# Performance work log

Hardware: AMD Instinct MI355X
Metric: run time of the kernel (lower is better)

The kernel has to match this reference:

```python
import jax, jax.numpy as jnp
import numpy as np

B, S, HID, NH = 8, 1024, 1024, 16
DH = HID // NH
ZERO = 1e-8  # undefined repo constant, assumed small epsilon


def setup_inputs() -> dict:
    key = jax.random.key(0)
    ks = jax.random.split(key, 14)
    sc = 1.0 / np.sqrt(HID)
    inp = {
        "Q": jax.random.normal(ks[0], (B, S, HID), jnp.float32),
        "K": jax.random.normal(ks[1], (B, S, HID), jnp.float32),
        "V": jax.random.normal(ks[2], (B, S, HID), jnp.float32),
        "Q_mask": jax.random.randint(ks[3], (B, S), 0, 2).astype(jnp.float32),
        "K_mask": jax.random.randint(ks[4], (B, S), 0, 2).astype(jnp.float32),
        "Wq": jax.random.normal(ks[5], (HID, HID), jnp.float32) * sc,
        "bq": jnp.zeros((HID,), jnp.float32),
        "Wk": jax.random.normal(ks[6], (HID, HID), jnp.float32) * sc,
        "bk": jnp.zeros((HID,), jnp.float32),
        "Wv": jax.random.normal(ks[7], (HID, HID), jnp.float32) * sc,
        "bv": jnp.zeros((HID,), jnp.float32),
        "Wo": jax.random.normal(ks[8], (HID, HID), jnp.float32) * sc,
        "bo": jnp.zeros((HID,), jnp.float32),
    }
    return inp


def _heads(x):  # [B,S,HID] -> [B,NH,S,DH]
    b, s, _ = x.shape
    return x.reshape(b, s, NH, DH).transpose(0, 2, 1, 3)


def reference(Q, K, V, Q_mask, K_mask, Wq, bq, Wk, bk, Wv, bv, Wo, bo):
    q = _heads(Q @ Wq.T + bq)
    k = _heads(K @ Wk.T + bk)
    v = _heads(V @ Wv.T + bv)
    # NOTE: original divides by head_size**(-0.5) == multiply by sqrt(DH)
    scores = jnp.einsum("bhqd,bhkd->bhqk", q, k) / (DH ** (-0.5))
    mask = Q_mask[:, :, None] * K_mask[:, None, :]  # [B,Sq,Sk]
    probs = jax.nn.softmax(scores, axis=-1)
    probs = jnp.where(mask[:, None, :, :] == 0, 0.0, probs)
    probs = probs / jnp.sum(probs + ZERO, axis=-1, keepdims=True)
    ctx = jnp.einsum("bhqk,bhkd->bqhd", probs, v).reshape(Q.shape[0], Q.shape[1], HID)
    return ctx @ Wo.T + bo
```

## Files before the change

### kernel.cpp

```cpp
#include <hip/hip_runtime.h>
#include <math.h>

constexpr int Bc   = 8;
constexpr int Sc   = 1024;
constexpr int HIDc = 1024;
constexpr int NHc  = 16;
constexpr int DHc  = 64;
constexpr int Mc   = Bc * Sc;
constexpr int Kc2  = 1024;
constexpr float SCALE    = 8.0f;
constexpr float EPS_TERM = 1024.0f * 1e-8f;

typedef short s16x8 __attribute__((ext_vector_type(8)));
typedef float f32x4 __attribute__((ext_vector_type(4)));

__device__ __forceinline__ ushort f2bf(float f) {
  unsigned u = __float_as_uint(f);
  u += 0x7FFFu + ((u >> 16) & 1u);
  return (ushort)(u >> 16);
}
__device__ __forceinline__ float bf2f(ushort h) {
  return __uint_as_float(((unsigned)h) << 16);
}
__device__ __forceinline__ unsigned pk2bf(float a, float b) {
  return (unsigned)f2bf(a) | ((unsigned)f2bf(b) << 16);
}

__device__ __forceinline__ void gl_lds16(const ushort* g, ushort* l) {
  __builtin_amdgcn_global_load_lds(
      (const __attribute__((address_space(1))) void*)g,
      (__attribute__((address_space(3))) void*)l, 16, 0, 0);
}

__device__ __forceinline__ void split8(const float4 v0, const float4 v1,
                                       s16x8& hi, s16x8& lo) {
  const float f[8] = {v0.x, v0.y, v0.z, v0.w, v1.x, v1.y, v1.z, v1.w};
  ushort h[8], l[8];
#pragma unroll
  for (int i = 0; i < 8; i++) {
    h[i] = f2bf(f[i]);
    l[i] = f2bf(f[i] - bf2f(h[i]));
  }
#pragma unroll
  for (int i = 0; i < 8; i++) { hi[i] = (short)h[i]; lo[i] = (short)l[i]; }
}

__global__ __launch_bounds__(256) void cvt_weights(
    const float4* __restrict__ Wq, const float4* __restrict__ Wk,
    const float4* __restrict__ Wv, const float4* __restrict__ Wo,
    ushort4* __restrict__ Wqh, ushort4* __restrict__ Wql,
    ushort4* __restrict__ Wkh, ushort4* __restrict__ Wkl,
    ushort4* __restrict__ Wvh, ushort4* __restrict__ Woh, int n4w)
{
  const int bpseg = n4w / 256;
  const int seg   = blockIdx.x / bpseg;
  const int li    = (blockIdx.x - seg * bpseg) * 256 + threadIdx.x;
  if (li >= n4w) return;
  if (seg == 0) {
    const float4 v = Wq[li];
    ushort4 h, l;
    h.x = f2bf(v.x); l.x = f2bf(v.x - bf2f(h.x));
    h.y = f2bf(v.y); l.y = f2bf(v.y - bf2f(h.y));
    h.z = f2bf(v.z); l.z = f2bf(v.z - bf2f(h.z));
    h.w = f2bf(v.w); l.w = f2bf(v.w - bf2f(h.w));
    Wqh[li] = h; Wql[li] = l;
  } else if (seg == 1) {
    const float4 v = Wk[li];
    ushort4 h, l;
    h.x = f2bf(v.x); l.x = f2bf(v.x - bf2f(h.x));
    h.y = f2bf(v.y); l.y = f2bf(v.y - bf2f(h.y));
    h.z = f2bf(v.z); l.z = f2bf(v.z - bf2f(h.z));
    h.w = f2bf(v.w); l.w = f2bf(v.w - bf2f(h.w));
    Wkh[li] = h; Wkl[li] = l;
  } else {
    const float4 v = (seg == 2) ? Wv[li] : Wo[li];
    ushort4 h;
    h.x = f2bf(v.x); h.y = f2bf(v.y); h.z = f2bf(v.z); h.w = f2bf(v.w);
    if (seg == 2) Wvh[li] = h; else Woh[li] = h;
  }
}

__global__ __launch_bounds__(256, 3) void qkv_gemm(
    const float* __restrict__ Qf, const float* __restrict__ Kf,
    const float* __restrict__ Vf,
    const ushort* __restrict__ Wqh, const ushort* __restrict__ Wql,
    const ushort* __restrict__ Wkh, const ushort* __restrict__ Wkl,
    const ushort* __restrict__ Wvh,
    const float* __restrict__ bq, const float* __restrict__ bk,
    const float* __restrict__ bv,
    ushort* __restrict__ qhi, ushort* __restrict__ qlo,
    ushort* __restrict__ khi, ushort* __restrict__ klo,
    ushort* __restrict__ vt)
{
  __shared__ ushort AhL[4096];
  __shared__ ushort BhL[4096];
  __shared__ ushort AlL[4096];
  __shared__ ushort BlL[4096];

  const int z = blockIdx.z;
  const bool split = (z < 2);
  const float*  Af = (z == 0) ? Qf : (z == 1) ? Kf : Vf;
  const ushort* Bh = (z == 0) ? Wqh : (z == 1) ? Wkh : Wvh;
  const ushort* Bl = (z == 0) ? Wql : Wkl;
  const float* bias = (z == 0) ? bq : (z == 1) ? bk : bv;

  const int t    = threadIdx.x;
  const int w    = t >> 6;
  const int ln   = t & 63;
  const int col  = ln & 15;
  const int quad = ln >> 4;
  const int wm   = w >> 1, wn = w & 1;
  const int m0   = blockIdx.y * 128;
  const int n0   = blockIdx.x * 128;

  f32x4 acc[4][4] = {};

  const int sA = w * 128;

  for (int k0 = 0; k0 < Kc2; k0 += 32) {
    float4 av[2][2];
#pragma unroll
    for (int j = 0; j < 2; j++) {
      const int s = sA + j * 64 + ln;
      const int r = s & 127, c = s >> 7;
      const float4* ga = (const float4*)(Af + (size_t)(m0 + r) * Kc2 + k0 + c * 8);
      av[j][0] = ga[0];
      av[j][1] = ga[1];
    }

    __syncthreads();

#pragma unroll
    for (int j = 0; j < 2; j++) {
      const int s = sA + j * 64 + ln;
      const int r = s & 127, c = s >> 7;
      const size_t goB = (size_t)(n0 + r) * Kc2 + k0 + c * 8;
      gl_lds16(Bh + goB, &BhL[(size_t)(sA + j * 64) * 8]);
      if (split) gl_lds16(Bl + goB, &BlL[(size_t)(sA + j * 64) * 8]);
    }
#pragma unroll
    for (int j = 0; j < 2; j++) {
      const int s = sA + j * 64 + ln;
      s16x8 hi, lo;
      split8(av[j][0], av[j][1], hi, lo);
      *(s16x8*)&AhL[(size_t)s * 8] = hi;
      if (split) *(s16x8*)&AlL[(size_t)s * 8] = lo;
    }
    __syncthreads();

    s16x8 a_h[4], b_h[4], a_l[4], b_l[4];
#pragma unroll
    for (int i = 0; i < 4; i++) {
      const int ai = (quad * 128 + wm * 64 + i * 16 + col) * 8;
      const int bi = (quad * 128 + wn * 64 + i * 16 + col) * 8;
      a_h[i] = *(const s16x8*)&AhL[ai];
      b_h[i] = *(const s16x8*)&BhL[bi];
      if (split) {
        a_l[i] = *(const s16x8*)&AlL[ai];
        b_l[i] = *(const s16x8*)&BlL[bi];
      }
    }
#pragma unroll
    for (int i = 0; i < 4; i++)
#pragma unroll
      for (int jj = 0; jj < 4; jj++) {
        acc[i][jj] = __builtin_amdgcn_mfma_f32_16x16x32_bf16(a_h[i], b_h[jj], acc[i][jj], 0, 0, 0);
        if (split) {
          acc[i][jj] = __builtin_amdgcn_mfma_f32_16x16x32_bf16(a_h[i], b_l[jj], acc[i][jj], 0, 0, 0);
          acc[i][jj] = __builtin_amdgcn_mfma_f32_16x16x32_bf16(a_l[i], b_h[jj], acc[i][jj], 0, 0, 0);
        }
      }
  }

  const int mb = m0 + wm * 64;
  const int nb = n0 + wn * 64;
  ushort* Ch = (z == 0) ? qhi : khi;
  ushort* Cl = (z == 0) ? qlo : klo;
#pragma unroll
  for (int i = 0; i < 4; i++)
#pragma unroll
    for (int jj = 0; jj < 4; jj++) {
      const int n  = nb + jj * 16 + col;
      const float bvv = bias[n];
#pragma unroll
      for (int r = 0; r < 4; r++) {
        const int m   = mb + i * 16 + quad * 4 + r;
        const float v = acc[i][jj][r] + bvv;
        const int b_ = m >> 10, s = m & (Sc - 1);
        const int h_ = n >> 6,  d = n & (DHc - 1);
        if (split) {
          const size_t off = (((size_t)b_ * NHc + h_) * Sc + s) * DHc + d;
          const ushort hb = f2bf(v);
          Ch[off] = hb;
          Cl[off] = f2bf(v - bf2f(hb));
        } else {
          const size_t off = (((size_t)b_ * NHc + h_) * DHc + d) * Sc + s;
          vt[off] = f2bf(v);
        }
      }
    }
}

__global__ __launch_bounds__(256, 3) void o_gemm(
    const ushort* __restrict__ Ag, const ushort* __restrict__ Bg,
    const float* __restrict__ bias, float* __restrict__ C)
{
  __shared__ ushort AhL[4096];
  __shared__ ushort BhL[4096];

  const int t    = threadIdx.x;
  const int w    = t >> 6;
  const int ln   = t & 63;
  const int col  = ln & 15;
  const int quad = ln >> 4;
  const int wm   = w >> 1, wn = w & 1;
  const int m0   = blockIdx.y * 128;
  const int n0   = blockIdx.x * 128;

  f32x4 acc[4][4] = {};
  const int sA = w * 128;

  for (int k0 = 0; k0 < Kc2; k0 += 32) {
    __syncthreads();
#pragma unroll
    for (int j = 0; j < 2; j++) {
      const int s = sA + j * 64 + ln;
      const int r = s & 127, c = s >> 7;
      gl_lds16(Ag + (size_t)(m0 + r) * Kc2 + k0 + c * 8, &AhL[(size_t)(sA + j * 64) * 8]);
      gl_lds16(Bg + (size_t)(n0 + r) * Kc2 + k0 + c * 8, &BhL[(size_t)(sA + j * 64) * 8]);
    }
    __syncthreads();

    s16x8 a_h[4], b_h[4];
#pragma unroll
    for (int i = 0; i < 4; i++) {
      a_h[i] = *(const s16x8*)&AhL[(quad * 128 + wm * 64 + i * 16 + col) * 8];
      b_h[i] = *(const s16x8*)&BhL[(quad * 128 + wn * 64 + i * 16 + col) * 8];
    }
#pragma unroll
    for (int i = 0; i < 4; i++)
#pragma unroll
      for (int jj = 0; jj < 4; jj++)
        acc[i][jj] = __builtin_amdgcn_mfma_f32_16x16x32_bf16(a_h[i], b_h[jj], acc[i][jj], 0, 0, 0);
  }

  const int mb = m0 + wm * 64;
  const int nb = n0 + wn * 64;
#pragma unroll
  for (int i = 0; i < 4; i++)
#pragma unroll
    for (int jj = 0; jj < 4; jj++) {
      const int n  = nb + jj * 16 + col;
      const float bvv = bias[n];
#pragma unroll
      for (int r = 0; r < 4; r++) {
        const int m = mb + i * 16 + quad * 4 + r;
        C[(size_t)m * HIDc + n] = acc[i][jj][r] + bvv;
      }
    }
}

constexpr int LDP = 72;

__global__ __launch_bounds__(256, 4) void attn_mfma(
    const ushort* __restrict__ qhi, const ushort* __restrict__ qlo,
    const ushort* __restrict__ khi, const ushort* __restrict__ klo,
    const ushort* __restrict__ vt,  const float* __restrict__ Qm,
    const float* __restrict__ Km,   ushort* __restrict__ ctx)
{
  __shared__ ushort KhiL[4096];
  __shared__ ushort KloL[4096];
  __shared__ ushort VtL [4096];
  __shared__ ushort PmL [64 * LDP];
  __shared__ float  kmL[64];

  const int t    = threadIdx.x;
  const int w    = t >> 6;
  const int ln   = t & 63;
  const int col  = ln & 15;
  const int quad = ln >> 4;

  const int id  = blockIdx.x;
  const int xcd = id & 7;
  const int j   = id >> 3;
  const int bh  = xcd * 16 + (j >> 4);
  const int qt  = j & 15;
  const int b   = bh >> 4;
  const int h   = bh & 15;

  const int qbase = qt * 64 + w * 16;
  const size_t headoff = (size_t)bh * Sc * DHc;

  s16x8 qh0, qh1, ql0, ql1;
  {
    const size_t ro = headoff + (size_t)(qbase + col) * DHc + quad * 8;
    qh0 = *(const s16x8*)(qhi + ro);
    qh1 = *(const s16x8*)(qhi + ro + 32);
    ql0 = *(const s16x8*)(qlo + ro);
    ql1 = *(const s16x8*)(qlo + ro + 32);
  }

  f32x4 OT[4] = {{0,0,0,0},{0,0,0,0},{0,0,0,0},{0,0,0,0}};
  float mrow = -INFINITY;
  float Zp = 0.0f, Zmp = 0.0f;

  for (int k0 = 0; k0 < Sc; k0 += 64) {
    __syncthreads();
#pragma unroll
    for (int jj = 0; jj < 2; jj++) {
      const int c = jj * 4 + w;
      const size_t gk = headoff + (size_t)(k0 + ln) * DHc + c * 8;
      const size_t gv = headoff + (size_t)ln * Sc + k0 + c * 8;
      gl_lds16(khi + gk, &KhiL[c * 512]);
      gl_lds16(klo + gk, &KloL[c * 512]);
      gl_lds16(vt  + gv, &VtL [c * 512]);
    }
    if (t < 64) kmL[t] = Km[b * Sc + k0 + t];
    __syncthreads();

    float s[4][4];
#pragma unroll
    for (int ks = 0; ks < 4; ks++) {
      const int base0 = (quad * 64 + ks * 16 + col) * 8;
      const int base1 = ((quad + 4) * 64 + ks * 16 + col) * 8;
      const s16x8 kh0 = *(const s16x8*)&KhiL[base0];
      const s16x8 kh1 = *(const s16x8*)&KhiL[base1];
      const s16x8 kl0 = *(const s16x8*)&KloL[base0];
      const s16x8 kl1 = *(const s16x8*)&KloL[base1];
      f32x4 a = {0,0,0,0};
      a = __builtin_amdgcn_mfma_f32_16x16x32_bf16(kh0, qh0, a, 0, 0, 0);
      a = __builtin_amdgcn_mfma_f32_16x16x32_bf16(kh1, qh1, a, 0, 0, 0);
      a = __builtin_amdgcn_mfma_f32_16x16x32_bf16(kh0, ql0, a, 0, 0, 0);
      a = __builtin_amdgcn_mfma_f32_16x16x32_bf16(kh1, ql1, a, 0, 0, 0);
      a = __builtin_amdgcn_mfma_f32_16x16x32_bf16(kl0, qh0, a, 0, 0, 0);
      a = __builtin_amdgcn_mfma_f32_16x16x32_bf16(kl1, qh1, a, 0, 0, 0);
#pragma unroll
      for (int r = 0; r < 4; r++) s[ks][r] = a[r] * SCALE;
    }

    float tmax = s[0][0];
#pragma unroll
    for (int ks = 0; ks < 4; ks++)
#pragma unroll
      for (int r = 0; r < 4; r++) tmax = fmaxf(tmax, s[ks][r]);
    tmax = fmaxf(tmax, __shfl_xor(tmax, 16, 64));
    tmax = fmaxf(tmax, __shfl_xor(tmax, 32, 64));

    const float mn    = fmaxf(mrow, tmax);
    const float alpha = __expf(mrow - mn);
    mrow = mn;

    float ps = 0.0f, pms = 0.0f;
    const int prow = (w * 16 + col) * LDP;
#pragma unroll
    for (int ks = 0; ks < 4; ks++) {
      const float4 km4 = *(const float4*)&kmL[ks * 16 + quad * 4];
      const float p0 = __expf(s[ks][0] - mn), p1 = __expf(s[ks][1] - mn);
      const float p2 = __expf(s[ks][2] - mn), p3 = __expf(s[ks][3] - mn);
      const float q0 = p0 * km4.x, q1 = p1 * km4.y, q2 = p2 * km4.z, q3 = p3 * km4.w;
      ps  += (p0 + p1) + (p2 + p3);
      pms += (q0 + q1) + (q2 + q3);
      uint2 pv;
      pv.x = pk2bf(q0, q1);
      pv.y = pk2bf(q2, q3);
      *(uint2*)&PmL[prow + ks * 16 + quad * 4] = pv;
    }
    Zp  = Zp  * alpha + ps;
    Zmp = Zmp * alpha + pms;
#pragma unroll
    for (int dt = 0; dt < 4; dt++) OT[dt] *= alpha;

    const s16x8 p0 = *(const s16x8*)&PmL[prow + quad * 8];
    const s16x8 p1 = *(const s16x8*)&PmL[prow + 32 + quad * 8];
#pragma unroll
    for (int dt = 0; dt < 4; dt++) {
      const s16x8 a0 = *(const s16x8*)&VtL[(quad * 64 + dt * 16 + col) * 8];
      const s16x8 a1 = *(const s16x8*)&VtL[((quad + 4) * 64 + dt * 16 + col) * 8];
      OT[dt] = __builtin_amdgcn_mfma_f32_16x16x32_bf16(a0, p0, OT[dt], 0, 0, 0);
      OT[dt] = __builtin_amdgcn_mfma_f32_16x16x32_bf16(a1, p1, OT[dt], 0, 0, 0);
    }
  }

  Zp  += __shfl_xor(Zp,  16, 64);  Zp  += __shfl_xor(Zp,  32, 64);
  Zmp += __shfl_xor(Zmp, 16, 64);  Zmp += __shfl_xor(Zmp, 32, 64);

  const int q     = qbase + col;
  const float qmv = Qm[b * Sc + q];
  const float rden = (qmv != 0.0f) ? 1.0f / (Zmp + EPS_TERM * Zp) : 0.0f;

  ushort* crow = ctx + (size_t)(b * Sc + q) * HIDc + h * DHc + quad * 4;
#pragma unroll
  for (int dt = 0; dt < 4; dt++) {
    uint2 ov;
    ov.x = pk2bf(OT[dt][0] * rden, OT[dt][1] * rden);
    ov.y = pk2bf(OT[dt][2] * rden, OT[dt][3] * rden);
    *(uint2*)(crow + dt * 16) = ov;
  }
}

extern "C" void kernel_launch(void* const* d_in, const int* in_sizes, int n_in,
                              void* d_out, int out_size, void* d_ws, size_t ws_size,
                              hipStream_t stream)
{
  const float* Q  = (const float*)d_in[0];
  const float* K  = (const float*)d_in[1];
  const float* V  = (const float*)d_in[2];
  const float* Qm = (const float*)d_in[3];
  const float* Km = (const float*)d_in[4];
  const float* Wq = (const float*)d_in[5];
  const float* bq = (const float*)d_in[6];
  const float* Wk = (const float*)d_in[7];
  const float* bk = (const float*)d_in[8];
  const float* Wv = (const float*)d_in[9];
  const float* bv = (const float*)d_in[10];
  const float* Wo = (const float*)d_in[11];
  const float* bo = (const float*)d_in[12];
  float* out = (float*)d_out;

  const size_t NEL = (size_t)Mc * HIDc;
  const size_t WEL = (size_t)HIDc * HIDc;

  ushort* Wqh = (ushort*)d_ws;
  ushort* Wql = Wqh + WEL;
  ushort* Wkh = Wql + WEL;
  ushort* Wkl = Wkh + WEL;
  ushort* Wvh = Wkl + WEL;
  ushort* Woh = Wvh + WEL;
  ushort* qhi = Woh + WEL;
  ushort* qlo = qhi + NEL;
  ushort* khi = qlo + NEL;
  ushort* klo = khi + NEL;
  ushort* vt  = klo + NEL;
  ushort* ctx = vt  + NEL;

  const int n4w = (int)(WEL / 4);

  cvt_weights<<<4 * (n4w / 256), 256, 0, stream>>>(
      (const float4*)Wq, (const float4*)Wk, (const float4*)Wv, (const float4*)Wo,
      (ushort4*)Wqh, (ushort4*)Wql, (ushort4*)Wkh, (ushort4*)Wkl,
      (ushort4*)Wvh, (ushort4*)Woh, n4w);

  dim3 gqkv(HIDc / 128, Mc / 128, 3);
  qkv_gemm<<<gqkv, 256, 0, stream>>>(Q, K, V,
      Wqh, Wql, Wkh, Wkl, Wvh, bq, bk, bv, qhi, qlo, khi, klo, vt);

  attn_mfma<<<Bc * NHc * (Sc / 64), 256, 0, stream>>>(qhi, qlo, khi, klo, vt, Qm, Km, ctx);

  dim3 gg(HIDc / 128, Mc / 128);
  o_gemm<<<gg, 256, 0, stream>>>(ctx, Woh, bo, out);
}
```

Measured before the change: 524.2 us.

## Switch attention and output GEMM to fp16, drop K low split, remap blocks

Q/K/V projection outputs, attention probabilities, context and Wo now use fp16 instead of bf16. K is stored as a single fp16 value, so the K-low buffer and two of the six score MFMAs per step are removed, which also cuts LDS use and global loads. Occupancy is raised to 6 blocks per CU. The QKV and O GEMM grids are flattened to 1-D with a swizzled block-to-tile mapping that spreads work across XCDs. The risk is fp16 overflow or precision loss in scores and outputs, which a split-K scheme previously protected against.

```diff
diff --git a/kernel.cpp b/kernel.cpp
--- a/kernel.cpp
+++ b/kernel.cpp
@@ -22,8 +22,16 @@
 __device__ __forceinline__ float bf2f(ushort h) {
   return __uint_as_float(((unsigned)h) << 16);
 }
-__device__ __forceinline__ unsigned pk2bf(float a, float b) {
-  return (unsigned)f2bf(a) | ((unsigned)f2bf(b) << 16);
+__device__ __forceinline__ ushort f2h(float f) {
+  _Float16 h = (_Float16)f;
+  return *(ushort*)&h;
+}
+__device__ __forceinline__ float h2f(ushort u) {
+  _Float16 h = *(_Float16*)&u;
+  return (float)h;
+}
+__device__ __forceinline__ unsigned pk2h(float a, float b) {
+  return (unsigned)f2h(a) | ((unsigned)f2h(b) << 16);
 }
 
 __device__ __forceinline__ void gl_lds16(const ushort* g, ushort* l) {
@@ -72,11 +80,16 @@
     h.z = f2bf(v.z); l.z = f2bf(v.z - bf2f(h.z));
     h.w = f2bf(v.w); l.w = f2bf(v.w - bf2f(h.w));
     Wkh[li] = h; Wkl[li] = l;
-  } else {
-    const float4 v = (seg == 2) ? Wv[li] : Wo[li];
+  } else if (seg == 2) {
+    const float4 v = Wv[li];
     ushort4 h;
     h.x = f2bf(v.x); h.y = f2bf(v.y); h.z = f2bf(v.z); h.w = f2bf(v.w);
-    if (seg == 2) Wvh[li] = h; else Woh[li] = h;
+    Wvh[li] = h;
+  } else {
+    const float4 v = Wo[li];
+    ushort4 h;
+    h.x = f2h(v.x); h.y = f2h(v.y); h.z = f2h(v.z); h.w = f2h(v.w);
+    Woh[li] = h;
   }
 }
 
@@ -89,15 +102,20 @@
     const float* __restrict__ bq, const float* __restrict__ bk,
     const float* __restrict__ bv,
     ushort* __restrict__ qhi, ushort* __restrict__ qlo,
-    ushort* __restrict__ khi, ushort* __restrict__ klo,
-    ushort* __restrict__ vt)
+    ushort* __restrict__ kf,  ushort* __restrict__ vt)
 {
   __shared__ ushort AhL[4096];
   __shared__ ushort BhL[4096];
   __shared__ ushort AlL[4096];
   __shared__ ushort BlL[4096];
 
-  const int z = blockIdx.z;
+  const int lin = blockIdx.x;
+  const int wk  = (lin & 7) * 192 + (lin >> 3);
+  const int z   = wk >> 9;
+  const int rem = wk & 511;
+  const int m0  = (rem >> 3) * 128;
+  const int n0  = (rem & 7) * 128;
+
   const bool split = (z < 2);
   const float*  Af = (z == 0) ? Qf : (z == 1) ? Kf : Vf;
   const ushort* Bh = (z == 0) ? Wqh : (z == 1) ? Wkh : Wvh;
@@ -110,11 +128,8 @@
   const int col  = ln & 15;
   const int quad = ln >> 4;
   const int wm   = w >> 1, wn = w & 1;
-  const int m0   = blockIdx.y * 128;
-  const int n0   = blockIdx.x * 128;
 
   f32x4 acc[4][4] = {};
-
   const int sA = w * 128;
 
   for (int k0 = 0; k0 < Kc2; k0 += 32) {
@@ -174,8 +189,6 @@
 
   const int mb = m0 + wm * 64;
   const int nb = n0 + wn * 64;
-  ushort* Ch = (z == 0) ? qhi : khi;
-  ushort* Cl = (z == 0) ? qlo : klo;
 #pragma unroll
   for (int i = 0; i < 4; i++)
 #pragma unroll
@@ -188,14 +201,17 @@
         const float v = acc[i][jj][r] + bvv;
         const int b_ = m >> 10, s = m & (Sc - 1);
         const int h_ = n >> 6,  d = n & (DHc - 1);
-        if (split) {
+        if (z == 0) {
           const size_t off = (((size_t)b_ * NHc + h_) * Sc + s) * DHc + d;
-          const ushort hb = f2bf(v);
-          Ch[off] = hb;
-          Cl[off] = f2bf(v - bf2f(hb));
+          const ushort hb = f2h(v);
+          qhi[off] = hb;
+          qlo[off] = f2h(v - h2f(hb));
+        } else if (z == 1) {
+          const size_t off = (((size_t)b_ * NHc + h_) * Sc + s) * DHc + d;
+          kf[off] = f2h(v);
         } else {
           const size_t off = (((size_t)b_ * NHc + h_) * DHc + d) * Sc + s;
-          vt[off] = f2bf(v);
+          vt[off] = f2h(v);
         }
       }
     }
@@ -208,14 +224,17 @@
   __shared__ ushort AhL[4096];
   __shared__ ushort BhL[4096];
 
+  const int lin = blockIdx.x;
+  const int wk  = (lin & 7) * 64 + (lin >> 3);
+  const int m0  = (wk >> 3) * 128;
+  const int n0  = (wk & 7) * 128;
+
   const int t    = threadIdx.x;
   const int w    = t >> 6;
   const int ln   = t & 63;
   const int col  = ln & 15;
   const int quad = ln >> 4;
   const int wm   = w >> 1, wn = w & 1;
-  const int m0   = blockIdx.y * 128;
-  const int n0   = blockIdx.x * 128;
 
   f32x4 acc[4][4] = {};
   const int sA = w * 128;
@@ -241,7 +260,7 @@
     for (int i = 0; i < 4; i++)
 #pragma unroll
       for (int jj = 0; jj < 4; jj++)
-        acc[i][jj] = __builtin_amdgcn_mfma_f32_16x16x32_bf16(a_h[i], b_h[jj], acc[i][jj], 0, 0, 0);
+        acc[i][jj] = __builtin_amdgcn_mfma_f32_16x16x32_f16(a_h[i], b_h[jj], acc[i][jj], 0, 0, 0);
   }
 
   const int mb = m0 + wm * 64;
@@ -262,16 +281,15 @@
 
 constexpr int LDP = 72;
 
-__global__ __launch_bounds__(256, 4) void attn_mfma(
+__global__ __launch_bounds__(256, 6) void attn_mfma(
     const ushort* __restrict__ qhi, const ushort* __restrict__ qlo,
-    const ushort* __restrict__ khi, const ushort* __restrict__ klo,
-    const ushort* __restrict__ vt,  const float* __restrict__ Qm,
-    const float* __restrict__ Km,   ushort* __restrict__ ctx)
+    const ushort* __restrict__ kf,  const ushort* __restrict__ vt,
+    const float* __restrict__ Qm,   const float* __restrict__ Km,
+    ushort* __restrict__ ctx)
 {
-  __shared__ ushort KhiL[4096];
-  __shared__ ushort KloL[4096];
-  __shared__ ushort VtL [4096];
-  __shared__ ushort PmL [64 * LDP];
+  __shared__ ushort KfL[4096];
+  __shared__ ushort VtL[4096];
+  __shared__ ushort PmL[64 * LDP];
   __shared__ float  kmL[64];
 
   const int t    = threadIdx.x;
@@ -311,9 +329,8 @@
       const int c = jj * 4 + w;
       const size_t gk = headoff + (size_t)(k0 + ln) * DHc + c * 8;
       const size_t gv = headoff + (size_t)ln * Sc + k0 + c * 8;
-      gl_lds16(khi + gk, &KhiL[c * 512]);
-      gl_lds16(klo + gk, &KloL[c * 512]);
-      gl_lds16(vt  + gv, &VtL [c * 512]);
+      gl_lds16(kf + gk, &KfL[c * 512]);
+      gl_lds16(vt + gv, &VtL[c * 512]);
     }
     if (t < 64) kmL[t] = Km[b * Sc + k0 + t];
     __syncthreads();
@@ -323,17 +340,13 @@
     for (int ks = 0; ks < 4; ks++) {
       const int base0 = (quad * 64 + ks * 16 + col) * 8;
       const int base1 = ((quad + 4) * 64 + ks * 16 + col) * 8;
-      const s16x8 kh0 = *(const s16x8*)&KhiL[base0];
-      const s16x8 kh1 = *(const s16x8*)&KhiL[base1];
-      const s16x8 kl0 = *(const s16x8*)&KloL[base0];
-      const s16x8 kl1 = *(const s16x8*)&KloL[base1];
+      const s16x8 k0f = *(const s16x8*)&KfL[base0];
+      const s16x8 k1f = *(const s16x8*)&KfL[base1];
       f32x4 a = {0,0,0,0};
-      a = __builtin_amdgcn_mfma_f32_16x16x32_bf16(kh0, qh0, a, 0, 0, 0);
-      a = __builtin_amdgcn_mfma_f32_16x16x32_bf16(kh1, qh1, a, 0, 0, 0);
-      a = __builtin_amdgcn_mfma_f32_16x16x32_bf16(kh0, ql0, a, 0, 0, 0);
-      a = __builtin_amdgcn_mfma_f32_16x16x32_bf16(kh1, ql1, a, 0, 0, 0);
-      a = __builtin_amdgcn_mfma_f32_16x16x32_bf16(kl0, qh0, a, 0, 0, 0);
-      a = __builtin_amdgcn_mfma_f32_16x16x32_bf16(kl1, qh1, a, 0, 0, 0);
+      a = __builtin_amdgcn_mfma_f32_16x16x32_f16(k0f, qh0, a, 0, 0, 0);
+      a = __builtin_amdgcn_mfma_f32_16x16x32_f16(k1f, qh1, a, 0, 0, 0);
+      a = __builtin_amdgcn_mfma_f32_16x16x32_f16(k0f, ql0, a, 0, 0, 0);
+      a = __builtin_amdgcn_mfma_f32_16x16x32_f16(k1f, ql1, a, 0, 0, 0);
 #pragma unroll
       for (int r = 0; r < 4; r++) s[ks][r] = a[r] * SCALE;
     }
@@ -361,8 +374,8 @@
       ps  += (p0 + p1) + (p2 + p3);
       pms += (q0 + q1) + (q2 + q3);
       uint2 pv;
-      pv.x = pk2bf(q0, q1);
-      pv.y = pk2bf(q2, q3);
+      pv.x = pk2h(q0, q1);
+      pv.y = pk2h(q2, q3);
       *(uint2*)&PmL[prow + ks * 16 + quad * 4] = pv;
     }
     Zp  = Zp  * alpha + ps;
@@ -376,8 +389,8 @@
     for (int dt = 0; dt < 4; dt++) {
       const s16x8 a0 = *(const s16x8*)&VtL[(quad * 64 + dt * 16 + col) * 8];
       const s16x8 a1 = *(const s16x8*)&VtL[((quad + 4) * 64 + dt * 16 + col) * 8];
-      OT[dt] = __builtin_amdgcn_mfma_f32_16x16x32_bf16(a0, p0, OT[dt], 0, 0, 0);
-      OT[dt] = __builtin_amdgcn_mfma_f32_16x16x32_bf16(a1, p1, OT[dt], 0, 0, 0);
+      OT[dt] = __builtin_amdgcn_mfma_f32_16x16x32_f16(a0, p0, OT[dt], 0, 0, 0);
+      OT[dt] = __builtin_amdgcn_mfma_f32_16x16x32_f16(a1, p1, OT[dt], 0, 0, 0);
     }
   }
 
@@ -392,8 +405,8 @@
 #pragma unroll
   for (int dt = 0; dt < 4; dt++) {
     uint2 ov;
-    ov.x = pk2bf(OT[dt][0] * rden, OT[dt][1] * rden);
-    ov.y = pk2bf(OT[dt][2] * rden, OT[dt][3] * rden);
+    ov.x = pk2h(OT[dt][0] * rden, OT[dt][1] * rden);
+    ov.y = pk2h(OT[dt][2] * rden, OT[dt][3] * rden);
     *(uint2*)(crow + dt * 16) = ov;
   }
 }
@@ -428,9 +441,8 @@
   ushort* Woh = Wvh + WEL;
   ushort* qhi = Woh + WEL;
   ushort* qlo = qhi + NEL;
-  ushort* khi = qlo + NEL;
-  ushort* klo = khi + NEL;
-  ushort* vt  = klo + NEL;
+  ushort* kf  = qlo + NEL;
+  ushort* vt  = kf  + NEL;
   ushort* ctx = vt  + NEL;
 
   const int n4w = (int)(WEL / 4);
@@ -440,12 +452,10 @@
       (ushort4*)Wqh, (ushort4*)Wql, (ushort4*)Wkh, (ushort4*)Wkl,
       (ushort4*)Wvh, (ushort4*)Woh, n4w);
 
-  dim3 gqkv(HIDc / 128, Mc / 128, 3);
-  qkv_gemm<<<gqkv, 256, 0, stream>>>(Q, K, V,
-      Wqh, Wql, Wkh, Wkl, Wvh, bq, bk, bv, qhi, qlo, khi, klo, vt);
-
-  attn_mfma<<<Bc * NHc * (Sc / 64), 256, 0, stream>>>(qhi, qlo, khi, klo, vt, Qm, Km, ctx);
-
-  dim3 gg(HIDc / 128, Mc / 128);
-  o_gemm<<<gg, 256, 0, stream>>>(ctx, Woh, bo, out);
-}
+  qkv_gemm<<<1536, 256, 0, stream>>>(Q, K, V,
+      Wqh, Wql, Wkh, Wkl, Wvh, bq, bk, bv, qhi, qlo, kf, vt);
+
+  attn_mfma<<<Bc * NHc * (Sc / 64), 256, 0, stream>>>(qhi, qlo, kf, vt, Qm, Km, ctx);
+
+  o_gemm<<<512, 256, 0, stream>>>(ctx, Woh, bo, out);
+}
```

Measured after the change: 571.3 us. 9.0% more time.
